# Kernel optimization log

Measured on AMD Instinct MI355X. Metric: run time of the kernel, lower is better.

## Reference

```python
import jax, jax.numpy as jnp
import numpy as np

N_NODES = 100000
N_EDGES = 1000000
D_IN = 64
D_OUT = 64


def setup_inputs() -> dict:
    key = jax.random.key(0)
    k1, k2, k3, k4 = jax.random.split(key, 4)
    x = jax.random.normal(k1, (N_NODES, D_IN), dtype=jnp.float32)
    edge_index = jax.random.randint(k2, (2, N_EDGES), 0, N_NODES, dtype=jnp.int64)
    edge_weight = jax.random.uniform(k3, (N_EDGES,), dtype=jnp.float32)
    W = jax.random.normal(k4, (D_OUT, D_IN), dtype=jnp.float32) * (1.0 / np.sqrt(D_IN))
    bias = jnp.zeros((D_OUT,), dtype=jnp.float32)
    return {"x": x, "edge_index": edge_index, "edge_weight": edge_weight, "W": W, "bias": bias}


def reference(x, edge_index, edge_weight, W, bias):
    n = x.shape[0]
    self_loops = jnp.arange(n)
    row = jnp.concatenate([edge_index[0], self_loops])  # [E+N]
    col = jnp.concatenate([edge_index[1], self_loops])  # [E+N]
    ew = jnp.concatenate([edge_weight, jnp.ones((n,), x.dtype)])  # [E+N]
    # degree via scatter-add of edge weights into row nodes
    deg = jax.ops.segment_sum(ew, row, num_segments=n)  # [N]
    deg_safe = jnp.where(deg > 0, deg, 1.0)
    deg_inv_sqrt = jnp.where(deg > 0, jax.lax.rsqrt(deg_safe), 0.0)  # inf -> 0
    norm = deg_inv_sqrt[row] * ew * deg_inv_sqrt[col]  # [E+N]
    # gather-scale-scatter aggregation
    msg = x[col] * norm[:, None]  # [E+N, D_IN]
    out = jax.ops.segment_sum(msg, row, num_segments=n)  # [N, D_IN]
    return out @ W.T + bias
```

## Files before the change

kernel.cpp:

```cpp
#include <hip/hip_runtime.h>
#include <hip/hip_bf16.h>

#define D 64
#define K 24
#define M44 ((1ULL << 44) - 1)
#define SPILLCAP 65536

typedef __attribute__((ext_vector_type(4))) _Float16 half4;
typedef __attribute__((ext_vector_type(8))) _Float16 half8;

__global__ __launch_bounds__(256) void k_build(const int* __restrict__ rowi,
                                               const int* __restrict__ coli,
                                               const float* __restrict__ ew,
                                               unsigned long long* __restrict__ packed,
                                               unsigned int* __restrict__ slots,
                                               int4* __restrict__ spill,
                                               int* __restrict__ spillCnt, int nE) {
    int b = blockIdx.x;
    int p = b & 7;
    int e = (b >> 3) * 256 + threadIdx.x;
    if (e >= nE) return;
    int r = rowi[e];
    if ((r & 7) != p) return;
    int c = coli[e];
    float w = ew[e];
    unsigned long long fx = (unsigned long long)((double)w * 4294967296.0);
    unsigned long long old = atomicAdd(&packed[r], (1ULL << 44) | fx);
    int rank = (int)(old >> 44);
    if (rank < K) {
        int q = (int)(w * 32768.0f + 0.5f);
        if (q > 32767) q = 32767;
        slots[r * K + rank] = ((unsigned int)c << 15) | (unsigned int)q;
    } else {
        int pI = atomicAdd(spillCnt, 1);
        if (pI < SPILLCAP) spill[pI] = make_int4(r, c, __float_as_int(w), 0);
    }
}

__global__ __launch_bounds__(256) void k_xhalf(const float4* __restrict__ x4,
                                               half8* __restrict__ xh8, int nv) {
    int t = blockIdx.x * 256 + threadIdx.x;
    if (t >= nv) return;
    float4 a = x4[2 * t], b = x4[2 * t + 1];
    half8 h;
    h[0] = (_Float16)a.x; h[1] = (_Float16)a.y; h[2] = (_Float16)a.z; h[3] = (_Float16)a.w;
    h[4] = (_Float16)b.x; h[5] = (_Float16)b.y; h[6] = (_Float16)b.z; h[7] = (_Float16)b.w;
    xh8[t] = h;
}

__device__ __forceinline__ float dis_of(unsigned long long pk) {
    return rsqrtf(1.0f + (float)(pk & M44) * (1.0f / 4294967296.0f));
}

template <bool H>
__global__ __launch_bounds__(256) void k_gather_gemm(const float* __restrict__ x,
                                                     const _Float16* __restrict__ xh,
                                                     const unsigned long long* __restrict__ packed,
                                                     const unsigned int* __restrict__ slots,
                                                     const int4* __restrict__ spill,
                                                     const int* __restrict__ spillCnt,
                                                     const float* __restrict__ W,
                                                     const float* __restrict__ bias,
                                                     float* __restrict__ out, int n) {
    __shared__ float Bs[D * D];
    __shared__ float Ast[16 * D];
    float4* Ast4 = (float4*)Ast;
    int tid = threadIdx.x;

    const float4* W4 = (const float4*)W;
#pragma unroll
    for (int v = 0; v < 4; ++v) {
        int idx = tid + v * 256;
        int o  = idx >> 4;
        int kc = idx & 15;
        float4 wv = W4[idx];
        int gq = o >> 2, oo = o & 3;
        int cpos = 4 * ((gq + kc) & 15) + oo;
        Bs[(4 * kc + 0) * 64 + cpos] = wv.x;
        Bs[(4 * kc + 1) * 64 + cpos] = wv.y;
        Bs[(4 * kc + 2) * 64 + cpos] = wv.z;
        Bs[(4 * kc + 3) * 64 + cpos] = wv.w;
    }

    int j   = tid & 15;
    int grp = tid >> 4;
    int i0  = blockIdx.x * 16;
    int i   = i0 + grp;

    float4 acc = make_float4(0.f, 0.f, 0.f, 0.f);
    const float4* x4 = (const float4*)x;
    const half4*  xh4 = (const half4*)xh;
    if (i < n) {
        unsigned long long pk = packed[i];
        int rawc = (int)(pk >> 44);
        int c_n = rawc < K ? rawc : K;
        int s = i * K;
        for (int off = 0; off < c_n; off += 16) {
            int idx = off + j;
            unsigned int rec = 0u;
            float wj = 0.f;
            if (idx < c_n) {
                rec = slots[s + idx];
                wj = (float)(rec & 32767u) * (1.0f / 32768.0f) * dis_of(packed[rec >> 15]);
            }
            int mm = c_n - off; if (mm > 16) mm = 16;
#pragma unroll
            for (int t = 0; t < 16; ++t) {
                if (t < mm) {
                    int col = (int)((unsigned int)__shfl((int)rec, t, 16) >> 15);
                    float w = __shfl(wj, t, 16);
                    if constexpr (H) {
                        half4 hv = xh4[col * 16 + j];
                        acc.x += w * (float)hv[0]; acc.y += w * (float)hv[1];
                        acc.z += w * (float)hv[2]; acc.w += w * (float)hv[3];
                    } else {
                        float4 xv = x4[col * 16 + j];
                        acc.x += w * xv.x; acc.y += w * xv.y;
                        acc.z += w * xv.z; acc.w += w * xv.w;
                    }
                }
            }
        }
        if (rawc > K) {
            int total = *spillCnt;
            if (total > SPILLCAP) total = SPILLCAP;
            for (int sp = 0; sp < total; ++sp) {
                int4 v = spill[sp];
                if (v.x == i) {
                    float w = __int_as_float(v.z) * dis_of(packed[v.y]);
                    if constexpr (H) {
                        half4 hv = xh4[v.y * 16 + j];
                        acc.x += w * (float)hv[0]; acc.y += w * (float)hv[1];
                        acc.z += w * (float)hv[2]; acc.w += w * (float)hv[3];
                    } else {
                        float4 xv = x4[v.y * 16 + j];
                        acc.x += w * xv.x; acc.y += w * xv.y;
                        acc.z += w * xv.z; acc.w += w * xv.w;
                    }
                }
            }
        }
        float di = dis_of(pk);
        if constexpr (H) {
            half4 hi = xh4[i * 16 + j];
            acc.x = di * (di * (float)hi[0] + acc.x);
            acc.y = di * (di * (float)hi[1] + acc.y);
            acc.z = di * (di * (float)hi[2] + acc.z);
            acc.w = di * (di * (float)hi[3] + acc.w);
        } else {
            float4 xi = x4[i * 16 + j];
            acc.x = di * (di * xi.x + acc.x);
            acc.y = di * (di * xi.y + acc.y);
            acc.z = di * (di * xi.z + acc.z);
            acc.w = di * (di * xi.w + acc.w);
        }
    }
    Ast4[grp * 16 + ((j + (grp >> 2)) & 15)] = acc;
    __syncthreads();

    int row = tid >> 4;
    int cg  = tid & 15;
    float4 oacc = ((const float4*)bias)[cg];
#pragma unroll 4
    for (int kc = 0; kc < 16; ++kc) {
        float4 a4 = Ast4[row * 16 + ((kc + (row >> 2)) & 15)];
        int cp = 4 * ((cg + kc) & 15);
        float4 b0 = *(const float4*)&Bs[(4 * kc + 0) * 64 + cp];
        float4 b1 = *(const float4*)&Bs[(4 * kc + 1) * 64 + cp];
        float4 b2 = *(const float4*)&Bs[(4 * kc + 2) * 64 + cp];
        float4 b3 = *(const float4*)&Bs[(4 * kc + 3) * 64 + cp];
        oacc.x += a4.x * b0.x + a4.y * b1.x + a4.z * b2.x + a4.w * b3.x;
        oacc.y += a4.x * b0.y + a4.y * b1.y + a4.z * b2.y + a4.w * b3.y;
        oacc.z += a4.x * b0.z + a4.y * b1.z + a4.z * b2.z + a4.w * b3.z;
        oacc.w += a4.x * b0.w + a4.y * b1.w + a4.z * b2.w + a4.w * b3.w;
    }
    int r = i0 + row;
    if (r < n) ((float4*)out)[r * 16 + cg] = oacc;
}

extern "C" void kernel_launch(void* const* d_in, const int* in_sizes, int n_in,
                              void* d_out, int out_size, void* d_ws, size_t ws_size,
                              hipStream_t stream) {
    const float* x    = (const float*)d_in[0];
    const int*   ei   = (const int*)d_in[1];
    const float* ew   = (const float*)d_in[2];
    const float* W    = (const float*)d_in[3];
    const float* bias = (const float*)d_in[4];
    float* out = (float*)d_out;

    int n  = in_sizes[0] / D;
    int nE = in_sizes[2];
    const int* rowi = ei;
    const int* coli = ei + nE;

    char* w = (char*)d_ws;
    unsigned long long* packed = (unsigned long long*)w; w += (size_t)n * 8;
    int* spillCnt = (int*)w;                             w += 64;
    unsigned int* slots = (unsigned int*)w;              w += (size_t)n * K * 4;
    int4* spill = (int4*)w;                              w += (size_t)SPILLCAP * 16;
    _Float16* xh = (_Float16*)w;

    size_t need = (size_t)n * 8 + 64 + (size_t)n * K * 4 + (size_t)SPILLCAP * 16
                + (size_t)n * D * 2;
    bool useH = ws_size >= need;

    int gE = (nE + 255) / 256;
    int gT = (n + 15) / 16;
    int nv = n * D / 8;

    hipMemsetAsync(packed, 0, (size_t)n * 8 + 64, stream);
    if (useH)
        k_xhalf<<<(nv + 255) / 256, 256, 0, stream>>>((const float4*)x, (half8*)xh, nv);
    k_build<<<gE * 8, 256, 0, stream>>>(rowi, coli, ew, packed, slots, spill, spillCnt, nE);
    if (useH)
        k_gather_gemm<true><<<gT, 256, 0, stream>>>(x, xh, packed, slots, spill, spillCnt, W, bias, out, n);
    else
        k_gather_gemm<false><<<gT, 256, 0, stream>>>(x, xh, packed, slots, spill, spillCnt, W, bias, out, n);
}
```

Baseline: 194.0 us.

## Fuse x-to-half and W transpose into build kernel; read W from global

```diff
diff --git a/kernel.cpp b/kernel.cpp
--- a/kernel.cpp
+++ b/kernel.cpp
@@ -8,6 +8,7 @@
 
 typedef __attribute__((ext_vector_type(4))) _Float16 half4;
 typedef __attribute__((ext_vector_type(8))) _Float16 half8;
+typedef __attribute__((ext_vector_type(4))) float f32x4;
 
 __global__ __launch_bounds__(256) void k_build(const int* __restrict__ rowi,
                                                const int* __restrict__ coli,
@@ -15,36 +16,48 @@
                                                unsigned long long* __restrict__ packed,
                                                unsigned int* __restrict__ slots,
                                                int4* __restrict__ spill,
-                                               int* __restrict__ spillCnt, int nE) {
+                                               int* __restrict__ spillCnt, int nE,
+                                               int buildBlocks,
+                                               const float4* __restrict__ x4,
+                                               half8* __restrict__ xh8, int nv,
+                                               const float* __restrict__ W,
+                                               float* __restrict__ Wt, int useH) {
     int b = blockIdx.x;
-    int p = b & 7;
-    int e = (b >> 3) * 256 + threadIdx.x;
-    if (e >= nE) return;
-    int r = rowi[e];
-    if ((r & 7) != p) return;
-    int c = coli[e];
-    float w = ew[e];
-    unsigned long long fx = (unsigned long long)((double)w * 4294967296.0);
-    unsigned long long old = atomicAdd(&packed[r], (1ULL << 44) | fx);
-    int rank = (int)(old >> 44);
-    if (rank < K) {
-        int q = (int)(w * 32768.0f + 0.5f);
-        if (q > 32767) q = 32767;
-        slots[r * K + rank] = ((unsigned int)c << 15) | (unsigned int)q;
-    } else {
-        int pI = atomicAdd(spillCnt, 1);
-        if (pI < SPILLCAP) spill[pI] = make_int4(r, c, __float_as_int(w), 0);
-    }
-}
-
-__global__ __launch_bounds__(256) void k_xhalf(const float4* __restrict__ x4,
-                                               half8* __restrict__ xh8, int nv) {
-    int t = blockIdx.x * 256 + threadIdx.x;
-    if (t >= nv) return;
-    float4 a = x4[2 * t], b = x4[2 * t + 1];
+    if (b < buildBlocks) {
+        int p = b & 7;
+        int e = (b >> 3) * 256 + threadIdx.x;
+        if (e >= nE) return;
+        int r = rowi[e];
+        if ((r & 7) != p) return;
+        int c = coli[e];
+        float w = ew[e];
+        unsigned long long fx = (unsigned long long)((double)w * 4294967296.0);
+        unsigned long long old = atomicAdd(&packed[r], (1ULL << 44) | fx);
+        int rank = (int)(old >> 44);
+        if (rank < K) {
+            int q = (int)(w * 32768.0f + 0.5f);
+            if (q > 32767) q = 32767;
+            slots[r * K + rank] = ((unsigned int)c << 15) | (unsigned int)q;
+        } else {
+            int pI = atomicAdd(spillCnt, 1);
+            if (pI < SPILLCAP) spill[pI] = make_int4(r, c, __float_as_int(w), 0);
+        }
+        return;
+    }
+    int pb = b - buildBlocks;
+    if (pb == 0) {
+        for (int idx = threadIdx.x; idx < D * D; idx += 256) {
+            int o = idx >> 6, k = idx & 63;
+            Wt[k * D + o] = W[idx];
+        }
+        return;
+    }
+    int t = (pb - 1) * 256 + threadIdx.x;
+    if (!useH || t >= nv) return;
+    float4 a = x4[2 * t], bb = x4[2 * t + 1];
     half8 h;
     h[0] = (_Float16)a.x; h[1] = (_Float16)a.y; h[2] = (_Float16)a.z; h[3] = (_Float16)a.w;
-    h[4] = (_Float16)b.x; h[5] = (_Float16)b.y; h[6] = (_Float16)b.z; h[7] = (_Float16)b.w;
+    h[4] = (_Float16)bb.x; h[5] = (_Float16)bb.y; h[6] = (_Float16)bb.z; h[7] = (_Float16)bb.w;
     xh8[t] = h;
 }
 
@@ -59,28 +72,12 @@
                                                      const unsigned int* __restrict__ slots,
                                                      const int4* __restrict__ spill,
                                                      const int* __restrict__ spillCnt,
-                                                     const float* __restrict__ W,
+                                                     const float* __restrict__ Wt,
                                                      const float* __restrict__ bias,
                                                      float* __restrict__ out, int n) {
-    __shared__ float Bs[D * D];
     __shared__ float Ast[16 * D];
     float4* Ast4 = (float4*)Ast;
     int tid = threadIdx.x;
-
-    const float4* W4 = (const float4*)W;
-#pragma unroll
-    for (int v = 0; v < 4; ++v) {
-        int idx = tid + v * 256;
-        int o  = idx >> 4;
-        int kc = idx & 15;
-        float4 wv = W4[idx];
-        int gq = o >> 2, oo = o & 3;
-        int cpos = 4 * ((gq + kc) & 15) + oo;
-        Bs[(4 * kc + 0) * 64 + cpos] = wv.x;
-        Bs[(4 * kc + 1) * 64 + cpos] = wv.y;
-        Bs[(4 * kc + 2) * 64 + cpos] = wv.z;
-        Bs[(4 * kc + 3) * 64 + cpos] = wv.w;
-    }
 
     int j   = tid & 15;
     int grp = tid >> 4;
@@ -100,7 +97,7 @@
             unsigned int rec = 0u;
             float wj = 0.f;
             if (idx < c_n) {
-                rec = slots[s + idx];
+                rec = __builtin_nontemporal_load(&slots[s + idx]);
                 wj = (float)(rec & 32767u) * (1.0f / 32768.0f) * dis_of(packed[rec >> 15]);
             }
             int mm = c_n - off; if (mm > 16) mm = 16;
@@ -160,22 +157,25 @@
 
     int row = tid >> 4;
     int cg  = tid & 15;
+    const float4* Wt4 = (const float4*)Wt;
     float4 oacc = ((const float4*)bias)[cg];
 #pragma unroll 4
     for (int kc = 0; kc < 16; ++kc) {
         float4 a4 = Ast4[row * 16 + ((kc + (row >> 2)) & 15)];
-        int cp = 4 * ((cg + kc) & 15);
-        float4 b0 = *(const float4*)&Bs[(4 * kc + 0) * 64 + cp];
-        float4 b1 = *(const float4*)&Bs[(4 * kc + 1) * 64 + cp];
-        float4 b2 = *(const float4*)&Bs[(4 * kc + 2) * 64 + cp];
-        float4 b3 = *(const float4*)&Bs[(4 * kc + 3) * 64 + cp];
+        float4 b0 = Wt4[(4 * kc + 0) * 16 + cg];
+        float4 b1 = Wt4[(4 * kc + 1) * 16 + cg];
+        float4 b2 = Wt4[(4 * kc + 2) * 16 + cg];
+        float4 b3 = Wt4[(4 * kc + 3) * 16 + cg];
         oacc.x += a4.x * b0.x + a4.y * b1.x + a4.z * b2.x + a4.w * b3.x;
         oacc.y += a4.x * b0.y + a4.y * b1.y + a4.z * b2.y + a4.w * b3.y;
         oacc.z += a4.x * b0.z + a4.y * b1.z + a4.z * b2.z + a4.w * b3.z;
         oacc.w += a4.x * b0.w + a4.y * b1.w + a4.z * b2.w + a4.w * b3.w;
     }
     int r = i0 + row;
-    if (r < n) ((float4*)out)[r * 16 + cg] = oacc;
+    if (r < n) {
+        f32x4 o4 = { oacc.x, oacc.y, oacc.z, oacc.w };
+        __builtin_nontemporal_store(o4, &((f32x4*)out)[r * 16 + cg]);
+    }
 }
 
 extern "C" void kernel_launch(void* const* d_in, const int* in_sizes, int n_in,
@@ -198,22 +198,25 @@
     int* spillCnt = (int*)w;                             w += 64;
     unsigned int* slots = (unsigned int*)w;              w += (size_t)n * K * 4;
     int4* spill = (int4*)w;                              w += (size_t)SPILLCAP * 16;
+    float* Wt = (float*)w;                               w += (size_t)D * D * 4;
     _Float16* xh = (_Float16*)w;
 
     size_t need = (size_t)n * 8 + 64 + (size_t)n * K * 4 + (size_t)SPILLCAP * 16
-                + (size_t)n * D * 2;
-    bool useH = ws_size >= need;
+                + (size_t)D * D * 4 + (size_t)n * D * 2;
+    int useH = ws_size >= need ? 1 : 0;
 
     int gE = (nE + 255) / 256;
+    int buildBlocks = gE * 8;
+    int nv = n * D / 8;
+    int prepBlocks = 1 + (useH ? (nv + 255) / 256 : 0);
     int gT = (n + 15) / 16;
-    int nv = n * D / 8;
 
     hipMemsetAsync(packed, 0, (size_t)n * 8 + 64, stream);
+    k_build<<<buildBlocks + prepBlocks, 256, 0, stream>>>(
+        rowi, coli, ew, packed, slots, spill, spillCnt, nE,
+        buildBlocks, (const float4*)x, (half8*)xh, nv, W, Wt, useH);
     if (useH)
-        k_xhalf<<<(nv + 255) / 256, 256, 0, stream>>>((const float4*)x, (half8*)xh, nv);
-    k_build<<<gE * 8, 256, 0, stream>>>(rowi, coli, ew, packed, slots, spill, spillCnt, nE);
-    if (useH)
-        k_gather_gemm<true><<<gT, 256, 0, stream>>>(x, xh, packed, slots, spill, spillCnt, W, bias, out, n);
+        k_gather_gemm<true><<<gT, 256, 0, stream>>>(x, xh, packed, slots, spill, spillCnt, Wt, bias, out, n);
     else
-        k_gather_gemm<false><<<gT, 256, 0, stream>>>(x, xh, packed, slots, spill, spillCnt, W, bias, out, n);
-}
+        k_gather_gemm<false><<<gT, 256, 0, stream>>>(x, xh, packed, slots, spill, spillCnt, Wt, bias, out, n);
+}
```

New measurement: 214.1 us. 1.1x slower.
